# Kernel optimization log

Measured on AMD Instinct MI355X. Metric: run time of the kernel, lower is better.

The kernel has to match this reference:

```python
import jax, jax.numpy as jnp
import numpy as np

N, D, E, B, NMAX, C = 50000, 64, 800000, 50, 1000, 100


def setup_inputs() -> dict:
    key = jax.random.key(0)
    ks = jax.random.split(key, 12)
    s = 0.05
    return {
        "x": jax.random.normal(ks[0], (N, D), jnp.float32),
        "e": jax.random.normal(ks[1], (E, D), jnp.float32),
        "edge_index": jax.random.randint(ks[2], (2, E), 0, N),
        "attr1": jax.random.normal(ks[3], (B, C, D), jnp.float32),
        "nc1": jax.random.uniform(ks[4], (B, NMAX, C), jnp.float32),
        "x_idx": jnp.arange(N),
        "eps1": jnp.zeros((1,), jnp.float32),
        "eps2": jnp.zeros((1,), jnp.float32),
        "W_ma": jax.random.normal(ks[5], (2 * D, D), jnp.float32) * s,
        "b_ma": jnp.zeros((D,), jnp.float32),
        "W_mu": jax.random.normal(ks[6], (D, D), jnp.float32) * s,
        "b_mu": jnp.zeros((D,), jnp.float32),
        "W_ua": jax.random.normal(ks[7], (D, D), jnp.float32) * s,
        "b_ua": jnp.zeros((D,), jnp.float32),
        "W_uu": jax.random.normal(ks[8], (D, D), jnp.float32) * s,
        "b_uu": jnp.zeros((D,), jnp.float32),
        "W_c": jax.random.normal(ks[9], (2 * D, D), jnp.float32) * s,
        "b_c": jnp.zeros((D,), jnp.float32),
    }


def reference(x, e, edge_index, attr1, nc1, x_idx, eps1, eps2,
              W_ma, b_ma, W_mu, b_mu, W_ua, b_ua, W_uu, b_uu, W_c, b_c):
    # adjacency branch: gather -> MLP -> scatter-sum (GIN-style)
    x_j = x[edge_index[0]]                                   # [E, D]
    msg_adj = jax.nn.relu(jnp.concatenate([x_j, e], axis=-1) @ W_ma + b_ma)
    agg_adj = jax.ops.segment_sum(msg_adj, edge_index[1], num_segments=x.shape[0])
    # hierarchical pooling branch: cluster MLP then dense matmul back to nodes
    msg_up = jax.nn.relu(attr1 @ W_mu + b_mu)                # [B, C, D]
    agg_up = jnp.einsum('bnc,bcd->bnd', nc1, msg_up)         # [B, NMAX, D]
    agg_up = agg_up.reshape(-1, agg_up.shape[-1])[x_idx]     # [N, D]
    out_adj = jax.nn.relu((agg_adj + (1.0 + eps1) * x) @ W_ua + b_ua)
    out_up = jax.nn.relu((agg_up + (1.0 + eps2) * x) @ W_uu + b_uu)
    return jnp.concatenate([out_adj, out_up], axis=-1) @ W_c + b_c
```

## Files before the change

### kernel.cpp

```cpp
#include <hip/hip_runtime.h>

#define NN 50000
#define DD 64
#define EE 800000
#define BB 50
#define NMAXX 1000
#define CC 100

#define NBKT 391
#define BCAP 3072

typedef short short8 __attribute__((ext_vector_type(8)));
typedef float float4v __attribute__((ext_vector_type(4)));

__device__ __forceinline__ float rl(float v, int l) {
  return __int_as_float(__builtin_amdgcn_readlane(__float_as_int(v), l));
}
__device__ __forceinline__ short f2bf(float f) {
  unsigned u = __float_as_uint(f);
  unsigned r = (u + 0x7fffu + ((u >> 16) & 1u)) >> 16;
  return (short)r;
}
__device__ __forceinline__ unsigned pack2(float a, float b) {
  return (unsigned)(unsigned short)f2bf(a) |
         ((unsigned)(unsigned short)f2bf(b) << 16);
}
__device__ __forceinline__ short8 pack8(const float* p) {
  union { unsigned u[4]; short8 s; } r;
  float4 v0 = *(const float4*)p;
  float4 v1 = *(const float4*)(p + 4);
  r.u[0] = pack2(v0.x, v0.y); r.u[1] = pack2(v0.z, v0.w);
  r.u[2] = pack2(v1.x, v1.y); r.u[3] = pack2(v1.z, v1.w);
  return r.s;
}


__global__ __launch_bounds__(256) void k_prep(
    const int* __restrict__ ei, const float* __restrict__ x,
    const float* __restrict__ attr1,
    const float* __restrict__ Wma, const float* __restrict__ Wmu,
    const float* __restrict__ bmu, const float* __restrict__ Wua,
    const float* __restrict__ Wuu, const float* __restrict__ Wc,
    int* __restrict__ bcnt, short* __restrict__ xb,
    uint2* __restrict__ sdeB, short* __restrict__ msgupT,
    short* __restrict__ WtF, short* __restrict__ WtF1,
    short* __restrict__ WtF2, short* __restrict__ WtF3) {
  const int tid = threadIdx.x;
  if (blockIdx.x < EE / 256) {
    const int i = blockIdx.x * 256 + tid;
    const int s = ei[i];
    const int d = ei[EE + i];
    const int bkt = d >> 7;
    int pos = atomicAdd(&bcnt[bkt * 16], 1);
    if (pos < BCAP)
      sdeB[(size_t)bkt * BCAP + pos] =
          make_uint2((unsigned)s | ((unsigned)d << 16), (unsigned)i);
    {
      float4 xv = *(const float4*)&x[(size_t)i * 4];
      ((uint2*)xb)[i] = make_uint2(pack2(xv.x, xv.y), pack2(xv.z, xv.w));
    }
    if (i < 8192) {
      int j = i & 7, lane = (i >> 3) & 63, cbks = i >> 9;
      int cb = cbks & 3, ks = cbks >> 2;
      int k = ks * 32 + (lane >> 4) * 8 + j;
      int n = cb * 16 + (lane & 15);
      WtF[i]  = f2bf(Wma[k * 64 + n]);
      WtF3[i] = f2bf(Wc[k * 64 + n]);
      if (i < 4096) {
        WtF1[i] = f2bf(Wua[k * 64 + n]);
        WtF2[i] = f2bf(Wuu[k * 64 + n]);
      }
    }
  } else {
    __shared__ float Wl[64 * 64];
    for (int i = tid; i < 64 * 64; i += 256) Wl[i] = Wmu[i];
    __syncthreads();
    const int lane = tid & 63;
    const int row = (blockIdx.x - EE / 256) * 4 + (tid >> 6);
    float a = attr1[(size_t)row * 64 + lane];
    float acc = bmu[lane];
#pragma unroll 8
    for (int k = 0; k < 64; ++k)
      acc = fmaf(rl(a, k), Wl[k * 64 + lane], acc);
    const int b = row / 100, c = row - b * 100;
    msgupT[(size_t)b * 6400 + lane * 100 + c] = f2bf(fmaxf(acc, 0.f));
  }
}

__global__ __launch_bounds__(256) void k_sort(
    const uint2* __restrict__ sdeB, const int* __restrict__ bcnt,
    uint2* __restrict__ sde) {
  __shared__ uint2 Eb[BCAP];
  __shared__ int lcnt[128];
  __shared__ int lpos[128];
  __shared__ int red[256];
  const int b = blockIdx.x, t = threadIdx.x;
  int acc = 0;
  for (int j = t; j < b; j += 256) acc += bcnt[j * 16];
  red[t] = acc;
  __syncthreads();
#pragma unroll
  for (int off = 128; off; off >>= 1) {
    if (t < off) red[t] += red[t + off];
    __syncthreads();
  }
  const int base = red[0];
  int n = bcnt[b * 16];
  if (n > BCAP) n = BCAP;
  if (t < 128) lcnt[t] = 0;
  __syncthreads();
  for (int i = t; i < n; i += 256) {
    uint2 v = sdeB[(size_t)b * BCAP + i];
    Eb[i] = v;
    atomicAdd(&lcnt[(v.x >> 16) & 127], 1);
  }
  __syncthreads();
  if (t < 128) {
    int ssum = 0;
    for (int j = 0; j < t; ++j) ssum += lcnt[j];
    lpos[t] = ssum;
  }
  __syncthreads();
  for (int i = t; i < n; i += 256) {
    uint2 v = Eb[i];
    int p = atomicAdd(&lpos[(v.x >> 16) & 127], 1);
    sde[base + p] = v;
  }
}

__global__ __launch_bounds__(256) void k_aggup(
    const float* __restrict__ nc1, const short* __restrict__ msgupT,
    float* __restrict__ aggup) {
  constexpr int LDA = 136;
  __shared__ float Ncf[64 * CC];
  __shared__ short A[64 * LDA];
  __shared__ short Wt[64 * LDA];
  const int b = blockIdx.x >> 4;
  const int tile = blockIdx.x & 15;
  const int i0 = tile * 64;
  const int tid = threadIdx.x;
  const float* ncb = nc1 + ((size_t)b * NMAXX + i0) * CC;
  for (int idx = tid; idx < 64 * CC; idx += 256) {
    int r = idx / CC;
    Ncf[idx] = (i0 + r < NMAXX) ? ncb[idx] : 0.f;
  }
  {
    const unsigned* src = (const unsigned*)(msgupT + (size_t)b * 6400);
    unsigned* dstw = (unsigned*)Wt;
    for (int i = tid; i < 64 * 50; i += 256) {
      int row = i / 50, cu = i - row * 50;
      dstw[row * 68 + cu] = src[i];
    }
    for (int i = tid; i < 64 * 14; i += 256) {
      int row = i / 14, cu = 50 + (i - row * 14);
      dstw[row * 68 + cu] = 0;
    }
  }
  __syncthreads();
  {
    const int row = tid >> 2, kp = tid & 3;
#pragma unroll
    for (int j = 0; j < 16; ++j) {
      int k = kp * 32 + 2 * j;
      unsigned u = 0;
      if (k < CC) {
        float2 v = *(const float2*)&Ncf[row * CC + k];
        u = pack2(v.x, v.y);
      }
      *(unsigned*)&A[row * LDA + k] = u;
    }
  }
  __syncthreads();
  const int lane = tid & 63;
  const int w = tid >> 6;
  const int m = lane & 15;
  const int koff = (lane >> 4) * 8;
  float4v acc[4];
#pragma unroll
  for (int cb = 0; cb < 4; ++cb) acc[cb] = (float4v)0.f;
#pragma unroll
  for (int ks = 0; ks < 4; ++ks) {
    short8 af = *(const short8*)&A[(w * 16 + m) * LDA + ks * 32 + koff];
#pragma unroll
    for (int cb = 0; cb < 4; ++cb) {
      short8 bf = *(const short8*)&Wt[(cb * 16 + m) * LDA + ks * 32 + koff];
      acc[cb] = __builtin_amdgcn_mfma_f32_16x16x32_bf16(af, bf, acc[cb], 0, 0, 0);
    }
  }
  const int rbase = (lane >> 4) * 4;
#pragma unroll
  for (int cb = 0; cb < 4; ++cb)
#pragma unroll
    for (int r = 0; r < 4; ++r) {
      int i = i0 + w * 16 + rbase + r;
      if (i < NMAXX)
        aggup[((size_t)b * NMAXX + i) * 64 + cb * 16 + m] = acc[cb][r];
    }
}

__global__ __launch_bounds__(256) void k_edge_mfma(
    const short* __restrict__ xb, const float* __restrict__ e,
    const uint2* __restrict__ sde, const short* __restrict__ WtF,
    const float* __restrict__ bma, float* __restrict__ agg) {
  __shared__ short WtL[8192];
  __shared__ float Cs[4][16][68];
  const int tid = threadIdx.x;
  const int nwg = gridDim.x;
  const int qq = nwg >> 3, rr = nwg & 7;
  const int xx = blockIdx.x & 7, oo = blockIdx.x >> 3;
  const int bid = (xx < rr ? xx * (qq + 1) : rr * (qq + 1) + (xx - rr) * qq) + oo;
  {
    const uint4* s = (const uint4*)WtF;
    uint4* d = (uint4*)WtL;
#pragma unroll
    for (int it = 0; it < 4; ++it) d[it * 256 + tid] = s[it * 256 + tid];
  }
  __syncthreads();
  const int lane = tid & 63;
  const int wv = tid >> 6;
  const int m = lane & 15;
  const int koff = (lane >> 4) * 8;
  float bias[4];
#pragma unroll
  for (int cb = 0; cb < 4; ++cb) bias[cb] = bma[cb * 16 + m];
  const int base = bid * 256 + wv * 64;
  int dprev = -1;
  float run = 0.f;
#pragma unroll
  for (int c4 = 0; c4 < 4; ++c4) {
    const int tb = base + c4 * 16;
    const uint2 v = sde[tb + m];
    const int src = (int)(v.x & 0xffffu);
    const int dst = (int)(v.x >> 16);
    const int eid = (int)v.y;
    short8 a0 = *(const short8*)(xb + (size_t)src * 64 + koff);
    short8 a1 = *(const short8*)(xb + (size_t)src * 64 + 32 + koff);
    const float* er = e + (size_t)eid * 64;
    short8 a2 = pack8(er + koff);
    short8 a3 = pack8(er + 32 + koff);
    float4v acc[4];
#pragma unroll
    for (int cb = 0; cb < 4; ++cb) acc[cb] = (float4v)0.f;
#pragma unroll
    for (int cb = 0; cb < 4; ++cb) {
      short8 b0 = *(const short8*)&WtL[((0 * 4 + cb) * 64 + lane) * 8];
      short8 b1 = *(const short8*)&WtL[((1 * 4 + cb) * 64 + lane) * 8];
      short8 b2 = *(const short8*)&WtL[((2 * 4 + cb) * 64 + lane) * 8];
      short8 b3 = *(const short8*)&WtL[((3 * 4 + cb) * 64 + lane) * 8];
      acc[cb] = __builtin_amdgcn_mfma_f32_16x16x32_bf16(a0, b0, acc[cb], 0, 0, 0);
      acc[cb] = __builtin_amdgcn_mfma_f32_16x16x32_bf16(a1, b1, acc[cb], 0, 0, 0);
      acc[cb] = __builtin_amdgcn_mfma_f32_16x16x32_bf16(a2, b2, acc[cb], 0, 0, 0);
      acc[cb] = __builtin_amdgcn_mfma_f32_16x16x32_bf16(a3, b3, acc[cb], 0, 0, 0);
    }
    const int rbase = (lane >> 4) * 4;
#pragma unroll
    for (int cb = 0; cb < 4; ++cb)
#pragma unroll
      for (int r = 0; r < 4; ++r)
        Cs[wv][rbase + r][cb * 16 + m] = fmaxf(acc[cb][r] + bias[cb], 0.f);
#pragma unroll
    for (int r = 0; r < 16; ++r) {
      int dr = __builtin_amdgcn_readlane(dst, r);
      float val = Cs[wv][r][lane];
      if (dr != dprev) {
        if (run != 0.f) atomicAdd(&agg[(size_t)dprev * 64 + lane], run);
        run = 0.f;
        dprev = dr;
      }
      run += val;
    }
  }
  if (run != 0.f) atomicAdd(&agg[(size_t)dprev * 64 + lane], run);
}

__global__ __launch_bounds__(256) void k_final(
    const float* __restrict__ x, const float* __restrict__ agg,
    const float* __restrict__ aggup, const int* __restrict__ xidx,
    const float* __restrict__ eps1, const float* __restrict__ eps2,
    const short* __restrict__ WtF1, const float* __restrict__ bua,
    const short* __restrict__ WtF2, const float* __restrict__ buu,
    const short* __restrict__ WtF3, const float* __restrict__ bc,
    float* __restrict__ out) {
  constexpr int LD1 = 72;
  constexpr int LD3 = 136;
  __shared__ short A1[64 * LD1];
  __shared__ short A2[64 * LD1];
  __shared__ short O[64 * LD3];
  const int tid = threadIdx.x;
  const float s1 = 1.f + eps1[0], s2 = 1.f + eps2[0];
  const int r0 = blockIdx.x * 64;
  {
    const int row = tid >> 2, kp = tid & 3;
    int g = r0 + row;
    if (g >= NN) g = NN - 1;
    const size_t xb_ = (size_t)g * 64 + kp * 16;
    const size_t ub = (size_t)xidx[g] * 64 + kp * 16;
#pragma unroll
    for (int j = 0; j < 4; ++j) {
      float4 xv = *(const float4*)&x[xb_ + j * 4];
      float4 av = *(const float4*)&agg[xb_ + j * 4];
      float4 uv = *(const float4*)&aggup[ub + j * 4];
      unsigned h1lo = pack2(av.x + s1 * xv.x, av.y + s1 * xv.y);
      unsigned h1hi = pack2(av.z + s1 * xv.z, av.w + s1 * xv.w);
      unsigned h2lo = pack2(uv.x + s2 * xv.x, uv.y + s2 * xv.y);
      unsigned h2hi = pack2(uv.z + s2 * xv.z, uv.w + s2 * xv.w);
      *(uint2*)&A1[row * LD1 + kp * 16 + j * 4] = make_uint2(h1lo, h1hi);
      *(uint2*)&A2[row * LD1 + kp * 16 + j * 4] = make_uint2(h2lo, h2hi);
    }
  }
  __syncthreads();
  const int lane = tid & 63;
  const int w = tid >> 6;
  const int m = lane & 15;
  const int koff = (lane >> 4) * 8;
  const int rbase = (lane >> 4) * 4;
  float4v acc1[4], acc2[4];
#pragma unroll
  for (int cb = 0; cb < 4; ++cb) { acc1[cb] = (float4v)0.f; acc2[cb] = (float4v)0.f; }
#pragma unroll
  for (int ks = 0; ks < 2; ++ks) {
    short8 a1 = *(const short8*)&A1[(w * 16 + m) * LD1 + ks * 32 + koff];
    short8 a2 = *(const short8*)&A2[(w * 16 + m) * LD1 + ks * 32 + koff];
#pragma unroll
    for (int cb = 0; cb < 4; ++cb) {
      short8 b1 = *(const short8*)&WtF1[((ks * 4 + cb) * 64 + lane) * 8];
      short8 b2 = *(const short8*)&WtF2[((ks * 4 + cb) * 64 + lane) * 8];
      acc1[cb] = __builtin_amdgcn_mfma_f32_16x16x32_bf16(a1, b1, acc1[cb], 0, 0, 0);
      acc2[cb] = __builtin_amdgcn_mfma_f32_16x16x32_bf16(a2, b2, acc2[cb], 0, 0, 0);
    }
  }
#pragma unroll
  for (int cb = 0; cb < 4; ++cb) {
    float bb1 = bua[cb * 16 + m];
    float bb2 = buu[cb * 16 + m];
#pragma unroll
    for (int r = 0; r < 4; ++r) {
      int rowL = w * 16 + rbase + r;
      O[rowL * LD3 + cb * 16 + m] = f2bf(fmaxf(acc1[cb][r] + bb1, 0.f));
      O[rowL * LD3 + 64 + cb * 16 + m] = f2bf(fmaxf(acc2[cb][r] + bb2, 0.f));
    }
  }
  __syncthreads();
  float4v acc3[4];
#pragma unroll
  for (int cb = 0; cb < 4; ++cb) acc3[cb] = (float4v)0.f;
#pragma unroll
  for (int ks = 0; ks < 4; ++ks) {
    short8 af = *(const short8*)&O[(w * 16 + m) * LD3 + ks * 32 + koff];
#pragma unroll
    for (int cb = 0; cb < 4; ++cb) {
      short8 bf = *(const short8*)&WtF3[((ks * 4 + cb) * 64 + lane) * 8];
      acc3[cb] = __builtin_amdgcn_mfma_f32_16x16x32_bf16(af, bf, acc3[cb], 0, 0, 0);
    }
  }
#pragma unroll
  for (int cb = 0; cb < 4; ++cb) {
    float bb = bc[cb * 16 + m];
#pragma unroll
    for (int r = 0; r < 4; ++r) {
      int g = r0 + w * 16 + rbase + r;
      if (g < NN)
        out[(size_t)g * 64 + cb * 16 + m] = acc3[cb][r] + bb;
    }
  }
}

extern "C" void kernel_launch(void* const* d_in, const int* in_sizes, int n_in,
                              void* d_out, int out_size, void* d_ws, size_t ws_size,
                              hipStream_t stream) {
  const float* x     = (const float*)d_in[0];
  const float* e     = (const float*)d_in[1];
  const int*   ei    = (const int*)d_in[2];
  const float* attr1 = (const float*)d_in[3];
  const float* nc1   = (const float*)d_in[4];
  const int*   xidx  = (const int*)d_in[5];
  const float* eps1  = (const float*)d_in[6];
  const float* eps2  = (const float*)d_in[7];
  const float* Wma   = (const float*)d_in[8];
  const float* bma   = (const float*)d_in[9];
  const float* Wmu   = (const float*)d_in[10];
  const float* bmu   = (const float*)d_in[11];
  const float* Wua   = (const float*)d_in[12];
  const float* bua   = (const float*)d_in[13];
  const float* Wuu   = (const float*)d_in[14];
  const float* buu   = (const float*)d_in[15];
  const float* Wc    = (const float*)d_in[16];
  const float* bc    = (const float*)d_in[17];
  float* out = (float*)d_out;

  float* agg    = (float*)d_ws;
  int*   bcnt   = (int*)(agg + (size_t)NN * 64);
  float* aggup  = (float*)(bcnt + NBKT * 16);
  short* msgupT = (short*)(aggup + (size_t)NN * 64);
  short* xbuf   = msgupT + (size_t)BB * 6400;
  uint2* sdeB   = (uint2*)(xbuf + (size_t)NN * 64);
  uint2* sde    = sdeB + (size_t)NBKT * BCAP;
  short* WtF    = (short*)(sde + EE);
  short* WtF1   = WtF + 8192;
  short* WtF2   = WtF1 + 4096;
  short* WtF3   = WtF2 + 4096;

  hipMemsetAsync(agg, 0,
                 (size_t)NN * 64 * sizeof(float) + NBKT * 16 * sizeof(int),
                 stream);
  k_prep<<<dim3(EE / 256 + BB * CC / 4), dim3(256), 0, stream>>>(
      ei, x, attr1, Wma, Wmu, bmu, Wua, Wuu, Wc,
      bcnt, xbuf, sdeB, msgupT, WtF, WtF1, WtF2, WtF3);
  k_sort<<<dim3(NBKT), dim3(256), 0, stream>>>(sdeB, bcnt, sde);
  k_aggup<<<dim3(BB * 16), dim3(256), 0, stream>>>(nc1, msgupT, aggup);
  k_edge_mfma<<<dim3(EE / 256), dim3(256), 0, stream>>>(
      xbuf, e, sde, WtF, bma, agg);
  k_final<<<dim3((NN + 63) / 64), dim3(256), 0, stream>>>(
      x, agg, aggup, xidx, eps1, eps2, WtF1, bua, WtF2, buu, WtF3, bc, out);
}
```

Baseline: 463.6 us.

## Split concat matmul into per-node and per-edge projections before the edge scatter

Uses the linearity of the concat-matmul to precompute x@W_top once per node and e@W_bottom once per edge in a new MFMA kernel, storing both as bf16. The edge kernel then only gathers two projected rows, adds the bias, applies ReLU and does the segmented scatter, with no MFMA work. This removes the per-edge x gathers into the MFMA and the in-loop bf16 packing. In exchange it adds a full bf16 write and gather-read of an E×64 intermediate, which is extra memory traffic, and it rounds pre-activations to bf16, adding numerical error.

```diff
diff --git a/kernel.cpp b/kernel.cpp
--- a/kernel.cpp
+++ b/kernel.cpp
@@ -33,16 +33,18 @@
   r.u[2] = pack2(v1.x, v1.y); r.u[3] = pack2(v1.z, v1.w);
   return r.s;
 }
+__device__ __forceinline__ float b2f(unsigned short u) {
+  return __uint_as_float((unsigned)u << 16);
+}
 
 
 __global__ __launch_bounds__(256) void k_prep(
-    const int* __restrict__ ei, const float* __restrict__ x,
-    const float* __restrict__ attr1,
+    const int* __restrict__ ei, const float* __restrict__ attr1,
     const float* __restrict__ Wma, const float* __restrict__ Wmu,
     const float* __restrict__ bmu, const float* __restrict__ Wua,
     const float* __restrict__ Wuu, const float* __restrict__ Wc,
-    int* __restrict__ bcnt, short* __restrict__ xb,
-    uint2* __restrict__ sdeB, short* __restrict__ msgupT,
+    int* __restrict__ bcnt, uint2* __restrict__ sdeB,
+    short* __restrict__ msgupT,
     short* __restrict__ WtF, short* __restrict__ WtF1,
     short* __restrict__ WtF2, short* __restrict__ WtF3) {
   const int tid = threadIdx.x;
@@ -55,10 +57,6 @@
     if (pos < BCAP)
       sdeB[(size_t)bkt * BCAP + pos] =
           make_uint2((unsigned)s | ((unsigned)d << 16), (unsigned)i);
-    {
-      float4 xv = *(const float4*)&x[(size_t)i * 4];
-      ((uint2*)xb)[i] = make_uint2(pack2(xv.x, xv.y), pack2(xv.z, xv.w));
-    }
     if (i < 8192) {
       int j = i & 7, lane = (i >> 3) & 63, cbks = i >> 9;
       int cb = cbks & 3, ks = cbks >> 2;
@@ -126,6 +124,98 @@
     int p = atomicAdd(&lpos[(v.x >> 16) & 127], 1);
     sde[base + p] = v;
   }
+}
+
+__global__ __launch_bounds__(256) void k_pe(
+    const float* __restrict__ e, const float* __restrict__ x,
+    const short* __restrict__ WtF,
+    unsigned short* __restrict__ Peg, unsigned short* __restrict__ Pxb) {
+  __shared__ __align__(16) unsigned short Cs[4][16 * 72];
+  const int tid = threadIdx.x;
+  const int lane = tid & 63, wv = tid >> 6;
+  const int m = lane & 15;
+  const int koff = (lane >> 4) * 8;
+  const int rbase = (lane >> 4) * 4;
+  const bool isx = blockIdx.x >= EE / 256;
+  const float* sp = isx ? x : e;
+  const int r0 = (isx ? (int)blockIdx.x - EE / 256 : (int)blockIdx.x) * 256 + wv * 64;
+  const int ksb = isx ? 0 : 2;
+  const int sr = lane >> 2, part = lane & 3;
+#pragma unroll
+  for (int t = 0; t < 4; ++t) {
+    int row = r0 + t * 16 + m;
+    if (isx && row >= NN) row = NN - 1;
+    const float* rp = sp + (size_t)row * 64;
+    short8 a0 = pack8(rp + koff);
+    short8 a1 = pack8(rp + 32 + koff);
+    float4v acc[4];
+#pragma unroll
+    for (int cb = 0; cb < 4; ++cb) acc[cb] = (float4v)0.f;
+#pragma unroll
+    for (int cb = 0; cb < 4; ++cb) {
+      short8 b0 = *(const short8*)&WtF[(((ksb + 0) * 4 + cb) * 64 + lane) * 8];
+      short8 b1 = *(const short8*)&WtF[(((ksb + 1) * 4 + cb) * 64 + lane) * 8];
+      acc[cb] = __builtin_amdgcn_mfma_f32_16x16x32_bf16(a0, b0, acc[cb], 0, 0, 0);
+      acc[cb] = __builtin_amdgcn_mfma_f32_16x16x32_bf16(a1, b1, acc[cb], 0, 0, 0);
+    }
+#pragma unroll
+    for (int cb = 0; cb < 4; ++cb)
+#pragma unroll
+      for (int r = 0; r < 4; ++r)
+        Cs[wv][(rbase + r) * 72 + cb * 16 + m] = (unsigned short)f2bf(acc[cb][r]);
+    uint4 w0 = *(const uint4*)&Cs[wv][sr * 72 + part * 16];
+    uint4 w1 = *(const uint4*)&Cs[wv][sr * 72 + part * 16 + 8];
+    const int drow = r0 + t * 16 + sr;
+    if (!isx) {
+      unsigned short* dp = Peg + (size_t)drow * 64 + part * 16;
+      *(uint4*)dp = w0;
+      *(uint4*)(dp + 8) = w1;
+    } else if (drow < NN) {
+      unsigned short* dp = Pxb + (size_t)drow * 64 + part * 16;
+      *(uint4*)dp = w0;
+      *(uint4*)(dp + 8) = w1;
+    }
+  }
+}
+
+__global__ __launch_bounds__(256) void k_edge(
+    const uint2* __restrict__ sde, const unsigned short* __restrict__ Peg,
+    const unsigned short* __restrict__ Pxb, const float* __restrict__ bma,
+    float* __restrict__ agg) {
+  const int lane = threadIdx.x & 63;
+  const int wv = threadIdx.x >> 6;
+  const int i0 = blockIdx.x * 1024 + wv * 256;
+  if (i0 >= EE) return;
+  const float bias = bma[lane];
+  int dprev = -1;
+  float run = 0.f;
+  for (int i = 0; i < 256; i += 8) {
+    const int p = i0 + i;
+    uint4 s0 = *(const uint4*)&sde[p];
+    uint4 s1 = *(const uint4*)&sde[p + 2];
+    uint4 s2 = *(const uint4*)&sde[p + 4];
+    uint4 s3 = *(const uint4*)&sde[p + 6];
+    const unsigned sd_[8] = {s0.x, s0.z, s1.x, s1.z, s2.x, s2.z, s3.x, s3.z};
+    const unsigned ei_[8] = {s0.y, s0.w, s1.y, s1.w, s2.y, s2.w, s3.y, s3.w};
+    float pe[8], px[8];
+#pragma unroll
+    for (int j = 0; j < 8; ++j) {
+      pe[j] = b2f(Peg[(size_t)ei_[j] * 64 + lane]);
+      px[j] = b2f(Pxb[(size_t)(sd_[j] & 0xffffu) * 64 + lane]);
+    }
+#pragma unroll
+    for (int j = 0; j < 8; ++j) {
+      const int dst = (int)(sd_[j] >> 16);
+      float val = fmaxf(px[j] + pe[j] + bias, 0.f);
+      if (dst != dprev) {
+        if (run != 0.f) atomicAdd(&agg[(size_t)dprev * 64 + lane], run);
+        run = 0.f;
+        dprev = dst;
+      }
+      run += val;
+    }
+  }
+  if (run != 0.f) atomicAdd(&agg[(size_t)dprev * 64 + lane], run);
 }
 
 __global__ __launch_bounds__(256) void k_aggup(
@@ -196,81 +286,6 @@
       if (i < NMAXX)
         aggup[((size_t)b * NMAXX + i) * 64 + cb * 16 + m] = acc[cb][r];
     }
-}
-
-__global__ __launch_bounds__(256) void k_edge_mfma(
-    const short* __restrict__ xb, const float* __restrict__ e,
-    const uint2* __restrict__ sde, const short* __restrict__ WtF,
-    const float* __restrict__ bma, float* __restrict__ agg) {
-  __shared__ short WtL[8192];
-  __shared__ float Cs[4][16][68];
-  const int tid = threadIdx.x;
-  const int nwg = gridDim.x;
-  const int qq = nwg >> 3, rr = nwg & 7;
-  const int xx = blockIdx.x & 7, oo = blockIdx.x >> 3;
-  const int bid = (xx < rr ? xx * (qq + 1) : rr * (qq + 1) + (xx - rr) * qq) + oo;
-  {
-    const uint4* s = (const uint4*)WtF;
-    uint4* d = (uint4*)WtL;
-#pragma unroll
-    for (int it = 0; it < 4; ++it) d[it * 256 + tid] = s[it * 256 + tid];
-  }
-  __syncthreads();
-  const int lane = tid & 63;
-  const int wv = tid >> 6;
-  const int m = lane & 15;
-  const int koff = (lane >> 4) * 8;
-  float bias[4];
-#pragma unroll
-  for (int cb = 0; cb < 4; ++cb) bias[cb] = bma[cb * 16 + m];
-  const int base = bid * 256 + wv * 64;
-  int dprev = -1;
-  float run = 0.f;
-#pragma unroll
-  for (int c4 = 0; c4 < 4; ++c4) {
-    const int tb = base + c4 * 16;
-    const uint2 v = sde[tb + m];
-    const int src = (int)(v.x & 0xffffu);
-    const int dst = (int)(v.x >> 16);
-    const int eid = (int)v.y;
-    short8 a0 = *(const short8*)(xb + (size_t)src * 64 + koff);
-    short8 a1 = *(const short8*)(xb + (size_t)src * 64 + 32 + koff);
-    const float* er = e + (size_t)eid * 64;
-    short8 a2 = pack8(er + koff);
-    short8 a3 = pack8(er + 32 + koff);
-    float4v acc[4];
-#pragma unroll
-    for (int cb = 0; cb < 4; ++cb) acc[cb] = (float4v)0.f;
-#pragma unroll
-    for (int cb = 0; cb < 4; ++cb) {
-      short8 b0 = *(const short8*)&WtL[((0 * 4 + cb) * 64 + lane) * 8];
-      short8 b1 = *(const short8*)&WtL[((1 * 4 + cb) * 64 + lane) * 8];
-      short8 b2 = *(const short8*)&WtL[((2 * 4 + cb) * 64 + lane) * 8];
-      short8 b3 = *(const short8*)&WtL[((3 * 4 + cb) * 64 + lane) * 8];
-      acc[cb] = __builtin_amdgcn_mfma_f32_16x16x32_bf16(a0, b0, acc[cb], 0, 0, 0);
-      acc[cb] = __builtin_amdgcn_mfma_f32_16x16x32_bf16(a1, b1, acc[cb], 0, 0, 0);
-      acc[cb] = __builtin_amdgcn_mfma_f32_16x16x32_bf16(a2, b2, acc[cb], 0, 0, 0);
-      acc[cb] = __builtin_amdgcn_mfma_f32_16x16x32_bf16(a3, b3, acc[cb], 0, 0, 0);
-    }
-    const int rbase = (lane >> 4) * 4;
-#pragma unroll
-    for (int cb = 0; cb < 4; ++cb)
-#pragma unroll
-      for (int r = 0; r < 4; ++r)
-        Cs[wv][rbase + r][cb * 16 + m] = fmaxf(acc[cb][r] + bias[cb], 0.f);
-#pragma unroll
-    for (int r = 0; r < 16; ++r) {
-      int dr = __builtin_amdgcn_readlane(dst, r);
-      float val = Cs[wv][r][lane];
-      if (dr != dprev) {
-        if (run != 0.f) atomicAdd(&agg[(size_t)dprev * 64 + lane], run);
-        run = 0.f;
-        dprev = dr;
-      }
-      run += val;
-    }
-  }
-  if (run != 0.f) atomicAdd(&agg[(size_t)dprev * 64 + lane], run);
 }
 
 __global__ __launch_bounds__(256) void k_final(
@@ -392,8 +407,9 @@
   int*   bcnt   = (int*)(agg + (size_t)NN * 64);
   float* aggup  = (float*)(bcnt + NBKT * 16);
   short* msgupT = (short*)(aggup + (size_t)NN * 64);
-  short* xbuf   = msgupT + (size_t)BB * 6400;
-  uint2* sdeB   = (uint2*)(xbuf + (size_t)NN * 64);
+  unsigned short* Pxb = (unsigned short*)(msgupT + (size_t)BB * 6400);
+  unsigned short* Peg = Pxb + (size_t)NN * 64;
+  uint2* sdeB   = (uint2*)(Peg + (size_t)EE * 64);
   uint2* sde    = sdeB + (size_t)NBKT * BCAP;
   short* WtF    = (short*)(sde + EE);
   short* WtF1   = WtF + 8192;
@@ -404,12 +420,14 @@
                  (size_t)NN * 64 * sizeof(float) + NBKT * 16 * sizeof(int),
                  stream);
   k_prep<<<dim3(EE / 256 + BB * CC / 4), dim3(256), 0, stream>>>(
-      ei, x, attr1, Wma, Wmu, bmu, Wua, Wuu, Wc,
-      bcnt, xbuf, sdeB, msgupT, WtF, WtF1, WtF2, WtF3);
+      ei, attr1, Wma, Wmu, bmu, Wua, Wuu, Wc,
+      bcnt, sdeB, msgupT, WtF, WtF1, WtF2, WtF3);
+  k_pe<<<dim3(EE / 256 + (NN + 255) / 256), dim3(256), 0, stream>>>(
+      e, x, WtF, Peg, Pxb);
   k_sort<<<dim3(NBKT), dim3(256), 0, stream>>>(sdeB, bcnt, sde);
   k_aggup<<<dim3(BB * 16), dim3(256), 0, stream>>>(nc1, msgupT, aggup);
-  k_edge_mfma<<<dim3(EE / 256), dim3(256), 0, stream>>>(
-      xbuf, e, sde, WtF, bma, agg);
+  k_edge<<<dim3((EE + 1023) / 1024), dim3(256), 0, stream>>>(
+      sde, Peg, Pxb, bma, agg);
   k_final<<<dim3((NN + 63) / 64), dim3(256), 0, stream>>>(
       x, agg, aggup, xidx, eps1, eps2, WtF1, bua, WtF2, buu, WtF3, bc, out);
 }
```

Result: slower. 529.4 us (+14.2%).

## Fuse sort into bucketed edge kernel with shared-memory scatter accumulation

Applied to the files above, without the earlier changes.

Removes the separate per-bucket sort kernel. The edge MLP kernel now runs one 512-thread workgroup per 128-node destination bucket and accumulates messages into a shared-memory tile with LDS atomics. The tile is then written straight to agg, so the large memset of agg and all global atomics go away. The cost is that only 391 workgroups run, giving less parallelism and possible load imbalance, and bucket overflow is still capped at BCAP.

```diff
diff --git a/kernel.cpp b/kernel.cpp
--- a/kernel.cpp
+++ b/kernel.cpp
@@ -24,14 +24,6 @@
 __device__ __forceinline__ unsigned pack2(float a, float b) {
   return (unsigned)(unsigned short)f2bf(a) |
          ((unsigned)(unsigned short)f2bf(b) << 16);
-}
-__device__ __forceinline__ short8 pack8(const float* p) {
-  union { unsigned u[4]; short8 s; } r;
-  float4 v0 = *(const float4*)p;
-  float4 v1 = *(const float4*)(p + 4);
-  r.u[0] = pack2(v0.x, v0.y); r.u[1] = pack2(v0.z, v0.w);
-  r.u[2] = pack2(v1.x, v1.y); r.u[3] = pack2(v1.z, v1.w);
-  return r.s;
 }
 
 
@@ -87,47 +79,6 @@
   }
 }
 
-__global__ __launch_bounds__(256) void k_sort(
-    const uint2* __restrict__ sdeB, const int* __restrict__ bcnt,
-    uint2* __restrict__ sde) {
-  __shared__ uint2 Eb[BCAP];
-  __shared__ int lcnt[128];
-  __shared__ int lpos[128];
-  __shared__ int red[256];
-  const int b = blockIdx.x, t = threadIdx.x;
-  int acc = 0;
-  for (int j = t; j < b; j += 256) acc += bcnt[j * 16];
-  red[t] = acc;
-  __syncthreads();
-#pragma unroll
-  for (int off = 128; off; off >>= 1) {
-    if (t < off) red[t] += red[t + off];
-    __syncthreads();
-  }
-  const int base = red[0];
-  int n = bcnt[b * 16];
-  if (n > BCAP) n = BCAP;
-  if (t < 128) lcnt[t] = 0;
-  __syncthreads();
-  for (int i = t; i < n; i += 256) {
-    uint2 v = sdeB[(size_t)b * BCAP + i];
-    Eb[i] = v;
-    atomicAdd(&lcnt[(v.x >> 16) & 127], 1);
-  }
-  __syncthreads();
-  if (t < 128) {
-    int ssum = 0;
-    for (int j = 0; j < t; ++j) ssum += lcnt[j];
-    lpos[t] = ssum;
-  }
-  __syncthreads();
-  for (int i = t; i < n; i += 256) {
-    uint2 v = Eb[i];
-    int p = atomicAdd(&lpos[(v.x >> 16) & 127], 1);
-    sde[base + p] = v;
-  }
-}
-
 __global__ __launch_bounds__(256) void k_aggup(
     const float* __restrict__ nc1, const short* __restrict__ msgupT,
     float* __restrict__ aggup) {
@@ -198,79 +149,92 @@
     }
 }
 
-__global__ __launch_bounds__(256) void k_edge_mfma(
+__global__ __launch_bounds__(512) void k_edge_bkt(
     const short* __restrict__ xb, const float* __restrict__ e,
-    const uint2* __restrict__ sde, const short* __restrict__ WtF,
-    const float* __restrict__ bma, float* __restrict__ agg) {
+    const uint2* __restrict__ sdeB, const int* __restrict__ bcnt,
+    const short* __restrict__ WtF, const float* __restrict__ bma,
+    float* __restrict__ agg) {
+  constexpr int AS = 66;
   __shared__ short WtL[8192];
-  __shared__ float Cs[4][16][68];
+  __shared__ float Acc[128 * AS];
   const int tid = threadIdx.x;
-  const int nwg = gridDim.x;
-  const int qq = nwg >> 3, rr = nwg & 7;
-  const int xx = blockIdx.x & 7, oo = blockIdx.x >> 3;
-  const int bid = (xx < rr ? xx * (qq + 1) : rr * (qq + 1) + (xx - rr) * qq) + oo;
+  const int b = blockIdx.x;
   {
     const uint4* s = (const uint4*)WtF;
     uint4* d = (uint4*)WtL;
-#pragma unroll
-    for (int it = 0; it < 4; ++it) d[it * 256 + tid] = s[it * 256 + tid];
-  }
+    d[tid] = s[tid];
+    d[512 + tid] = s[512 + tid];
+  }
+  for (int i = tid; i < 128 * AS; i += 512) Acc[i] = 0.f;
   __syncthreads();
   const int lane = tid & 63;
   const int wv = tid >> 6;
   const int m = lane & 15;
   const int koff = (lane >> 4) * 8;
+  const int rbase = (lane >> 4) * 4;
   float bias[4];
 #pragma unroll
   for (int cb = 0; cb < 4; ++cb) bias[cb] = bma[cb * 16 + m];
-  const int base = bid * 256 + wv * 64;
-  int dprev = -1;
-  float run = 0.f;
-#pragma unroll
-  for (int c4 = 0; c4 < 4; ++c4) {
-    const int tb = base + c4 * 16;
-    const uint2 v = sde[tb + m];
+  int n = bcnt[b * 16];
+  if (n > BCAP) n = BCAP;
+  const uint2* eb = sdeB + (size_t)b * BCAP;
+  const int nch = (n + 15) >> 4;
+  for (int c = wv; c < nch; c += 8) {
+    const int c0 = c * 16;
+    int idx = c0 + m;
+    if (idx >= n) idx = n - 1;
+    const uint2 v = eb[idx];
     const int src = (int)(v.x & 0xffffu);
-    const int dst = (int)(v.x >> 16);
-    const int eid = (int)v.y;
     short8 a0 = *(const short8*)(xb + (size_t)src * 64 + koff);
     short8 a1 = *(const short8*)(xb + (size_t)src * 64 + 32 + koff);
-    const float* er = e + (size_t)eid * 64;
-    short8 a2 = pack8(er + koff);
-    short8 a3 = pack8(er + 32 + koff);
+    const float* er = e + (size_t)v.y * 64 + koff;
+    float4 f0 = *(const float4*)er;
+    float4 f1 = *(const float4*)(er + 4);
+    float4 f2 = *(const float4*)(er + 32);
+    float4 f3 = *(const float4*)(er + 36);
+    union { unsigned u[4]; short8 s; } p2, p3;
+    p2.u[0] = pack2(f0.x, f0.y); p2.u[1] = pack2(f0.z, f0.w);
+    p2.u[2] = pack2(f1.x, f1.y); p2.u[3] = pack2(f1.z, f1.w);
+    p3.u[0] = pack2(f2.x, f2.y); p3.u[1] = pack2(f2.z, f2.w);
+    p3.u[2] = pack2(f3.x, f3.y); p3.u[3] = pack2(f3.z, f3.w);
     float4v acc[4];
 #pragma unroll
-    for (int cb = 0; cb < 4; ++cb) acc[cb] = (float4v)0.f;
-#pragma unroll
     for (int cb = 0; cb < 4; ++cb) {
+      acc[cb] = (float4v)(bias[cb]);
       short8 b0 = *(const short8*)&WtL[((0 * 4 + cb) * 64 + lane) * 8];
       short8 b1 = *(const short8*)&WtL[((1 * 4 + cb) * 64 + lane) * 8];
       short8 b2 = *(const short8*)&WtL[((2 * 4 + cb) * 64 + lane) * 8];
       short8 b3 = *(const short8*)&WtL[((3 * 4 + cb) * 64 + lane) * 8];
       acc[cb] = __builtin_amdgcn_mfma_f32_16x16x32_bf16(a0, b0, acc[cb], 0, 0, 0);
       acc[cb] = __builtin_amdgcn_mfma_f32_16x16x32_bf16(a1, b1, acc[cb], 0, 0, 0);
-      acc[cb] = __builtin_amdgcn_mfma_f32_16x16x32_bf16(a2, b2, acc[cb], 0, 0, 0);
-      acc[cb] = __builtin_amdgcn_mfma_f32_16x16x32_bf16(a3, b3, acc[cb], 0, 0, 0);
-    }
-    const int rbase = (lane >> 4) * 4;
+      acc[cb] = __builtin_amdgcn_mfma_f32_16x16x32_bf16(p2.s, b2, acc[cb], 0, 0, 0);
+      acc[cb] = __builtin_amdgcn_mfma_f32_16x16x32_bf16(p3.s, b3, acc[cb], 0, 0, 0);
+    }
+    const int dstv = (int)(v.x >> 16);
+    int drs[4]; bool oks[4];
+#pragma unroll
+    for (int r = 0; r < 4; ++r) {
+      drs[r] = __shfl(dstv, rbase + r) & 127;
+      oks[r] = (c0 + rbase + r) < n;
+    }
 #pragma unroll
     for (int cb = 0; cb < 4; ++cb)
 #pragma unroll
       for (int r = 0; r < 4; ++r)
-        Cs[wv][rbase + r][cb * 16 + m] = fmaxf(acc[cb][r] + bias[cb], 0.f);
-#pragma unroll
-    for (int r = 0; r < 16; ++r) {
-      int dr = __builtin_amdgcn_readlane(dst, r);
-      float val = Cs[wv][r][lane];
-      if (dr != dprev) {
-        if (run != 0.f) atomicAdd(&agg[(size_t)dprev * 64 + lane], run);
-        run = 0.f;
-        dprev = dr;
-      }
-      run += val;
-    }
-  }
-  if (run != 0.f) atomicAdd(&agg[(size_t)dprev * 64 + lane], run);
+        if (oks[r])
+          atomicAdd(&Acc[drs[r] * AS + cb * 16 + m], fmaxf(acc[cb][r], 0.f));
+  }
+  __syncthreads();
+  const int row0 = b << 7;
+  for (int i = tid; i < 2048; i += 512) {
+    const int row = i >> 4, sg = (i & 15) * 4;
+    const int g = row0 + row;
+    if (g < NN) {
+      float* dp = &agg[(size_t)g * 64 + sg];
+      const float* sp = &Acc[row * AS + sg];
+      dp[0] = sp[0]; dp[1] = sp[1]; dp[2] = sp[2]; dp[3] = sp[3];
+    }
+  }
 }
 
 __global__ __launch_bounds__(256) void k_final(
@@ -394,22 +358,18 @@
   short* msgupT = (short*)(aggup + (size_t)NN * 64);
   short* xbuf   = msgupT + (size_t)BB * 6400;
   uint2* sdeB   = (uint2*)(xbuf + (size_t)NN * 64);
-  uint2* sde    = sdeB + (size_t)NBKT * BCAP;
-  short* WtF    = (short*)(sde + EE);
+  short* WtF    = (short*)(sdeB + (size_t)NBKT * BCAP);
   short* WtF1   = WtF + 8192;
   short* WtF2   = WtF1 + 4096;
   short* WtF3   = WtF2 + 4096;
 
-  hipMemsetAsync(agg, 0,
-                 (size_t)NN * 64 * sizeof(float) + NBKT * 16 * sizeof(int),
-                 stream);
+  hipMemsetAsync(bcnt, 0, NBKT * 16 * sizeof(int), stream);
   k_prep<<<dim3(EE / 256 + BB * CC / 4), dim3(256), 0, stream>>>(
       ei, x, attr1, Wma, Wmu, bmu, Wua, Wuu, Wc,
       bcnt, xbuf, sdeB, msgupT, WtF, WtF1, WtF2, WtF3);
-  k_sort<<<dim3(NBKT), dim3(256), 0, stream>>>(sdeB, bcnt, sde);
   k_aggup<<<dim3(BB * 16), dim3(256), 0, stream>>>(nc1, msgupT, aggup);
-  k_edge_mfma<<<dim3(EE / 256), dim3(256), 0, stream>>>(
-      xbuf, e, sde, WtF, bma, agg);
+  k_edge_bkt<<<dim3(NBKT), dim3(512), 0, stream>>>(
+      xbuf, e, sdeB, bcnt, WtF, bma, agg);
   k_final<<<dim3((NN + 63) / 64), dim3(256), 0, stream>>>(
       x, agg, aggup, xidx, eps1, eps2, WtF1, bua, WtF2, buu, WtF3, bc, out);
 }
```

Result: slower. 712.7 us (+53.7%).
